# Optimization experiments

Measured on AMD Instinct MI355X. Metric: run time of the kernel, lower is better.

Reference implementation:

```python
import jax, jax.numpy as jnp
import numpy as np

N_EMBD = 2048
N_HEAD = 32
N_GROUPS = 8
HEAD_DIM = N_EMBD // N_HEAD
Q_PER_KV = N_HEAD // N_GROUPS
QKV_DIM = (Q_PER_KV + 2) * N_GROUPS * HEAD_DIM


def apply_rope(x, cos, sin):
    # x: [B, nH, T, hd]; cos/sin: [T, rot//2]
    B, nH, T, hd = x.shape
    rot = min(sin.shape[1] * 2, hd)
    half = rot // 2
    x_rot, x_pass = x[..., :rot], x[..., rot:]
    c = cos[:T, :half][None, None]  # [1,1,T,half]
    s = sin[:T, :half][None, None]
    x1, x2 = x_rot[..., :half], x_rot[..., half:]
    x1_ = x1 * c - x2 * s
    x2_ = x2 * c + x1 * s
    return jnp.concatenate([x1_, x2_, x_pass], axis=-1)


def setup_inputs() -> dict:
    key = jax.random.key(0)
    k1, k2, k3, k4, k5 = jax.random.split(key, 5)
    B, T = 2, 2048
    x = jax.random.normal(k1, (B, T, N_EMBD), dtype=jnp.float32)
    cos = jax.random.uniform(k2, (T, HEAD_DIM // 2), dtype=jnp.float32)
    sin = jax.random.uniform(k3, (T, HEAD_DIM // 2), dtype=jnp.float32)
    attn_w = jax.random.normal(k4, (QKV_DIM, N_EMBD), dtype=jnp.float32) * (1.0 / np.sqrt(N_EMBD))
    proj_w = jax.random.normal(k5, (N_EMBD, N_EMBD), dtype=jnp.float32) * (1.0 / np.sqrt(N_EMBD))
    return {"x": x, "cos": cos, "sin": sin, "attn_w": attn_w, "proj_w": proj_w}


def reference(x, cos, sin, attn_w, proj_w):
    B, T, E = x.shape
    qkv = jnp.einsum('bte,fe->btf', x, attn_w)  # [B,T,QKV_DIM]
    qkv = qkv.reshape(B, T, N_GROUPS, Q_PER_KV + 2, HEAD_DIM)
    q = qkv[:, :, :, :Q_PER_KV].reshape(B, T, N_HEAD, HEAD_DIM)
    k = qkv[:, :, :, Q_PER_KV]      # [B,T,G,hd]
    v = qkv[:, :, :, Q_PER_KV + 1]  # [B,T,G,hd]
    # [B, heads, T, hd] layout; GQA repeat_interleave of K/V to full head count
    q = q.transpose(0, 2, 1, 3)
    k = jnp.repeat(k.transpose(0, 2, 1, 3), Q_PER_KV, axis=1)
    v = jnp.repeat(v.transpose(0, 2, 1, 3), Q_PER_KV, axis=1)
    q = apply_rope(q, cos, sin)
    k = apply_rope(k, cos, sin)
    scale = 1.0 / np.sqrt(HEAD_DIM)
    att = jax.nn.softmax(jnp.einsum('bhqd,bhkd->bhqk', q, k) * scale, axis=-1)
    out = jnp.einsum('bhqk,bhkd->bhqd', att, v)  # [B,nH,T,hd]
    out = out.transpose(0, 2, 1, 3).reshape(B, T, N_HEAD * HEAD_DIM)
    return jnp.einsum('bte,fe->btf', out, proj_w)
```

## Files before the change

kernel.cpp:

```cpp
#include <hip/hip_runtime.h>

typedef unsigned short u16;
typedef unsigned int u32;
typedef __bf16 bf16x8 __attribute__((ext_vector_type(8)));
typedef float f32x4 __attribute__((ext_vector_type(4)));
typedef float f32x16 __attribute__((ext_vector_type(16)));
typedef unsigned int u32x4 __attribute__((ext_vector_type(4)));

__device__ __forceinline__ u16 f2bf(float f) {
    u32 u = __builtin_bit_cast(u32, f);
    u32 r = u + 0x7FFFu + ((u >> 16) & 1u);
    return (u16)(r >> 16);
}
__device__ __forceinline__ u32 pack_bf16(float v0, float v1) {
    u32 a = __builtin_bit_cast(u32, v0) + 0x8000u;
    u32 b = __builtin_bit_cast(u32, v1) + 0x8000u;
    return __builtin_amdgcn_perm(b, a, 0x07060302u);
}
__device__ __forceinline__ u32 cvtpk(float lo, float hi) {
    u32 r;
    asm("v_cvt_pk_bf16_f32 %0, %1, %2" : "=v"(r) : "v"(lo), "v"(hi));
    return r;
}
__device__ __forceinline__ void plswap(u32& a, u32& b) {
    asm("v_permlane32_swap_b32 %0, %1" : "+v"(a), "+v"(b));
}
__device__ __forceinline__ void gload16(const u16* g, u16* l) {
    __builtin_amdgcn_global_load_lds(
        (const __attribute__((address_space(1))) u32*)g,
        (__attribute__((address_space(3))) u32*)l, 16, 0, 0);
}

#define QSCALE 0.18033688011111793f


__global__ __launch_bounds__(256) void cvt3_kernel(const float* __restrict__ a, u16* __restrict__ ao,
                                                   const float* __restrict__ b, u16* __restrict__ bo,
                                                   const float* __restrict__ c, u16* __restrict__ co) {
    int i = blockIdx.x * 256 + threadIdx.x;
    const float* src; u16* dst; int idx;
    if (i < 2097152)       { src = a; dst = ao; idx = i; }
    else if (i < 3670016)  { src = b; dst = bo; idx = i - 2097152; }
    else                   { src = c; dst = co; idx = i - 3670016; }
    float4 f = reinterpret_cast<const float4*>(src)[idx];
    u32 lo = (u32)f2bf(f.x) | ((u32)f2bf(f.y) << 16);
    u32 hi = (u32)f2bf(f.z) | ((u32)f2bf(f.w) << 16);
    reinterpret_cast<uint2*>(dst)[idx] = make_uint2(lo, hi);
}

__global__ __launch_bounds__(512, 2) void gemm_qkv(const u16* __restrict__ A,
                                                   const u16* __restrict__ Bw,
                                                   const float* __restrict__ cosb,
                                                   const float* __restrict__ sinb,
                                                   u16* __restrict__ Qo,
                                                   u16* __restrict__ Ko,
                                                   u16* __restrict__ Vt) {
    __shared__ __align__(16) u16 As[2 * 2 * 128 * 64];
    __shared__ __align__(16) u16 Bs[2 * 2 * 128 * 64];
    const int tid = threadIdx.x;
    const int w = tid >> 6, lane = tid & 63;
    const int quad = lane >> 4, l15 = lane & 15;
    const int wr = w >> 2, wc = w & 3;
    const int m0 = blockIdx.x * 256, n0 = blockIdx.y * 256;
    const int K = 2048;
    const int rsub = lane >> 3;
    const int csrc = (lane & 7) ^ rsub;
    const int sx = (l15 & 7) << 3;
    const int c0 = (quad * 8) ^ sx;
    const int c1 = (32 + quad * 8) ^ sx;

    f32x4 acc[8][4];
#pragma unroll
    for (int a = 0; a < 8; a++)
#pragma unroll
        for (int b = 0; b < 4; b++) acc[a][b] = (f32x4){0.f, 0.f, 0.f, 0.f};

    auto stage = [&](const u16* g, int row0, int kk, u16* lds) {
#pragma unroll
        for (int i = 0; i < 2; i++)
            gload16(g + (size_t)(row0 + (i * 8 + w) * 8 + rsub) * K + kk + csrc * 8,
                    lds + (i * 8 + w) * 512);
    };

    stage(A,  m0,       0, &As[0]);
    stage(A,  m0 + 128, 0, &As[8192]);
    stage(Bw, n0,       0, &Bs[0]);
    stage(Bw, n0 + 128, 0, &Bs[8192]);
    asm volatile("s_waitcnt vmcnt(0)" ::: "memory");
    __builtin_amdgcn_s_barrier();

    for (int j = 0; j < 32; ++j) {
        const int cur = j & 1;
        const u16* Ab = &As[cur * 16384 + wr * 8192];
        const u16* Bb = &Bs[cur * 16384 + (wc >> 1) * 8192 + (wc & 1) * 4096];
        u16* Asn = &As[(cur ^ 1) * 16384];
        u16* Bsn = &Bs[(cur ^ 1) * 16384];
        const int kk2 = (j + 1) * 64;
        bf16x8 af[4][2];
#pragma unroll
        for (int q = 0; q < 4; ++q) {
            const int qm = q >> 1, qn = q & 1;
            if (qn == 0) {
#pragma unroll
                for (int fm = 0; fm < 4; fm++) {
                    af[fm][0] = *reinterpret_cast<const bf16x8*>(&Ab[(qm * 64 + fm * 16 + l15) * 64 + c0]);
                    af[fm][1] = *reinterpret_cast<const bf16x8*>(&Ab[(qm * 64 + fm * 16 + l15) * 64 + c1]);
                }
            }
            bf16x8 bfv[2][2];
#pragma unroll
            for (int fn = 0; fn < 2; fn++) {
                bfv[fn][0] = *reinterpret_cast<const bf16x8*>(&Bb[(qn * 32 + fn * 16 + l15) * 64 + c0]);
                bfv[fn][1] = *reinterpret_cast<const bf16x8*>(&Bb[(qn * 32 + fn * 16 + l15) * 64 + c1]);
            }
            if (j < 31) {
                if (q == 0)      { stage(A,  m0,       kk2, Asn); stage(A,  m0 + 128, kk2, Asn + 8192); }
                else if (q == 1) { stage(Bw, n0,       kk2, Bsn); stage(Bw, n0 + 128, kk2, Bsn + 8192); }
            }
            __builtin_amdgcn_s_barrier();
            __builtin_amdgcn_s_setprio(1);
#pragma unroll
            for (int fm = 0; fm < 4; fm++)
#pragma unroll
                for (int fn = 0; fn < 2; fn++) {
                    acc[qm * 4 + fm][qn * 2 + fn] = __builtin_amdgcn_mfma_f32_16x16x32_bf16(
                        af[fm][0], bfv[fn][0], acc[qm * 4 + fm][qn * 2 + fn], 0, 0, 0);
                    acc[qm * 4 + fm][qn * 2 + fn] = __builtin_amdgcn_mfma_f32_16x16x32_bf16(
                        af[fm][1], bfv[fn][1], acc[qm * 4 + fm][qn * 2 + fn], 0, 0, 0);
                }
            __builtin_amdgcn_s_setprio(0);
            if (q == 3 && j < 31) asm volatile("s_waitcnt vmcnt(0)" ::: "memory");
            __builtin_amdgcn_s_barrier();
        }
    }

    const int nw0 = n0 + wc * 64;
    const int G = nw0 / 384;
    const int slot = (nw0 % 384) / 64;
    const int bb = m0 >> 11;
    const int tb0 = (m0 & 2047) + wr * 128 + quad * 4;
    if (slot == 5) {
        u16* vbase = Vt + ((size_t)(bb * 8 + G)) * 131072;
        const int half_v = quad >> 1, jb = (quad & 1) * 4;
#pragma unroll
        for (int fm = 0; fm < 8; fm++) {
            const int trow = tb0 + fm * 16;
            const int sb = (trow >> 6) * 4096 + ((trow >> 4) & 3) * 512 + half_v * 256 + jb;
#pragma unroll
            for (int fn = 0; fn < 4; fn++) {
                const int dt = fn >> 1, dl = (fn & 1) * 16 + l15;
                uint2 pk;
                pk.x = pack_bf16(acc[fm][fn][0], acc[fm][fn][1]);
                pk.y = pack_bf16(acc[fm][fn][2], acc[fm][fn][3]);
                *reinterpret_cast<uint2*>(vbase + sb + dt * 2048 + dl * 8) = pk;
            }
        }
    } else {
        const float sc = (slot < 4) ? QSCALE : 1.0f;
        u16* obase = (slot < 4)
            ? Qo + ((size_t)(bb * 32 + G * 4 + slot)) * 131072
            : Ko + ((size_t)(bb * 8 + G)) * 131072;
        const int laneoff = (l15 >> 3) * 256 + (l15 & 7);
#pragma unroll
        for (int fm = 0; fm < 8; fm++) {
#pragma unroll
            for (int i = 0; i < 4; i++) {
                const int t = tb0 + fm * 16 + i;
                const int tb = (t >> 5) * 2048 + (t & 31) * 8 + laneoff;
#pragma unroll
                for (int fn = 0; fn < 2; fn++) {
                    const int dh = fn * 16 + l15;
                    float c = cosb[t * 32 + dh], s = sinb[t * 32 + dh];
                    float x1 = acc[fm][fn][i], x2 = acc[fm][fn + 2][i];
                    obase[tb + fn * 512]       = f2bf((x1 * c - x2 * s) * sc);
                    obase[tb + (fn + 2) * 512] = f2bf((x2 * c + x1 * s) * sc);
                }
            }
        }
    }
}

__global__ __launch_bounds__(256) void gemm_bt(const u16* __restrict__ A,
                                               const u16* __restrict__ Bw,
                                               float* __restrict__ Cf,
                                               int M, int N, int K) {
    __shared__ __align__(16) u16 As[2 * 128 * 32];
    __shared__ __align__(16) u16 Bs[2 * 128 * 32];
    const int tid = threadIdx.x;
    const int wave = tid >> 6, lane = tid & 63, quad = lane >> 4, l15 = lane & 15;
    const int wm = wave >> 1, wn = wave & 1;
    const int m0 = blockIdx.x * 128, n0 = blockIdx.y * 128;
    const int lrow = lane >> 2, lcol = (lane & 3) * 8;
    f32x4 acc[4][4];
#pragma unroll
    for (int a = 0; a < 4; a++)
#pragma unroll
        for (int b = 0; b < 4; b++) acc[a][b] = (f32x4){0.f, 0.f, 0.f, 0.f};
    for (int kk = 0; kk < K; kk += 64) {
        __syncthreads();
#pragma unroll
        for (int p = 0; p < 2; p++)
#pragma unroll
            for (int c = 0; c < 2; c++) {
                const int rA = wave * 32 + c * 16;
                gload16(A  + (size_t)(m0 + rA + lrow) * K + kk + p * 32 + lcol,
                        &As[p * 4096 + rA * 32]);
                gload16(Bw + (size_t)(n0 + rA + lrow) * K + kk + p * 32 + lcol,
                        &Bs[p * 4096 + rA * 32]);
            }
        __syncthreads();
#pragma unroll
        for (int p = 0; p < 2; p++) {
            bf16x8 af[4], bfr[4];
#pragma unroll
            for (int t = 0; t < 4; t++) {
                af[t]  = *reinterpret_cast<const bf16x8*>(
                    &As[p * 4096 + (wm * 64 + t * 16 + l15) * 32 + quad * 8]);
                bfr[t] = *reinterpret_cast<const bf16x8*>(
                    &Bs[p * 4096 + (wn * 64 + t * 16 + l15) * 32 + quad * 8]);
            }
#pragma unroll
            for (int tm = 0; tm < 4; tm++)
#pragma unroll
                for (int tn = 0; tn < 4; tn++)
                    acc[tm][tn] = __builtin_amdgcn_mfma_f32_16x16x32_bf16(af[tm], bfr[tn], acc[tm][tn], 0, 0, 0);
        }
    }
#pragma unroll
    for (int tm = 0; tm < 4; tm++) {
        const int r0 = m0 + wm * 64 + tm * 16 + quad * 4;
#pragma unroll
        for (int tn = 0; tn < 4; tn++) {
            const int c = n0 + wn * 64 + tn * 16 + l15;
#pragma unroll
            for (int i = 0; i < 4; i++) Cf[(size_t)(r0 + i) * N + c] = acc[tm][tn][i];
        }
    }
}

__global__ __launch_bounds__(256, 4) void attn(const u16* __restrict__ Q,
                                               const u16* __restrict__ Kg,
                                               const u16* __restrict__ Vt,
                                               u16* __restrict__ O) {
    __shared__ __align__(16) u16 Ks[3 * 4096];
    __shared__ __align__(16) u16 Vts[2 * 4096];
    const int tid = threadIdx.x, w = tid >> 6, lane = tid & 63;
    const int half = lane >> 5, l31 = lane & 31;
    const int q0 = blockIdx.x * 128;
    const int h = blockIdx.y, b = blockIdx.z, g = h >> 2;
    const u16* qfb = Q + ((size_t)(b * 32 + h)) * 131072;
    const u16* kfb = Kg + ((size_t)(b * 8 + g)) * 131072;
    const u16* vfb = Vt + ((size_t)(b * 8 + g)) * 131072;

    const int Tq = (q0 >> 6) + (w >> 1);
#pragma unroll
    for (int ks = 0; ks < 4; ks++)
        gload16(qfb + ((size_t)((Tq * 8 + (w & 1) * 4 + ks) * 64) + lane) * 8,
                Ks + (w * 4 + ks) * 512);
    __syncthreads();
    bf16x8 qf[4];
#pragma unroll
    for (int ks = 0; ks < 4; ks++)
        qf[ks] = *reinterpret_cast<const bf16x8*>(&Ks[(w * 4 + ks) * 512 + lane * 8]);
    __syncthreads();

    f32x16 Oa[2];
#pragma unroll
    for (int t = 0; t < 2; t++)
#pragma unroll
        for (int i = 0; i < 16; i++) Oa[t][i] = 0.f;
    float lsum = 0.f;

    auto stage_k = [&](int T, int bsel) {
        u16* kd = Ks + bsel * 4096;
#pragma unroll
        for (int i = 0; i < 2; i++) {
            const int s = w * 2 + i;
            gload16(kfb + ((size_t)((T * 8 + s) * 64) + lane) * 8, kd + s * 512);
        }
    };
    auto stage_v = [&](int T, int bsel) {
        u16* vd = Vts + bsel * 4096;
#pragma unroll
        for (int i = 0; i < 2; i++) {
            const int s = w * 2 + i;
            gload16(vfb + ((size_t)((T * 8 + s) * 64) + lane) * 8, vd + s * 512);
        }
    };
    auto qk = [&](f32x16 (&S)[2], const u16* Kb) {
#pragma unroll
        for (int kt = 0; kt < 2; kt++) {
#pragma unroll
            for (int i = 0; i < 16; i++) S[kt][i] = 0.f;
#pragma unroll
            for (int ks = 0; ks < 4; ks++) {
                bf16x8 kf = *reinterpret_cast<const bf16x8*>(&Kb[(kt * 4 + ks) * 512 + lane * 8]);
                S[kt] = __builtin_amdgcn_mfma_f32_32x32x16_bf16(kf, qf[ks], S[kt], 0, 0, 0);
            }
        }
    };

    stage_k(0, 0);
    stage_v(0, 0);
    stage_k(1, 1);
    __syncthreads();
    f32x16 Sa[2], Sb[2];
    __builtin_amdgcn_s_setprio(1);
    qk(Sa, Ks);
    __builtin_amdgcn_s_setprio(0);

    auto body = [&](int t, int bn, int bs, f32x16 (&Sc)[2], f32x16 (&Sn)[2],
                    const u16* Vb) {
        if (t < 31) stage_v(t + 1, (t + 1) & 1);
        if (t < 30) stage_k(t + 2, bs);
        float ps = 0.f;
        u32 pw[4][4];
#pragma unroll
        for (int kt = 0; kt < 2; kt++) {
            float pe[16];
#pragma unroll
            for (int r = 0; r < 16; r++) pe[r] = __builtin_amdgcn_exp2f(Sc[kt][r]);
#pragma unroll
            for (int r = 0; r < 4; r++)
                ps += (pe[r * 4 + 0] + pe[r * 4 + 1]) + (pe[r * 4 + 2] + pe[r * 4 + 3]);
#pragma unroll
            for (int j = 0; j < 2; j++) {
                u32 X0 = cvtpk(pe[j * 8 + 0], pe[j * 8 + 1]);
                u32 Y0 = cvtpk(pe[j * 8 + 4], pe[j * 8 + 5]);
                u32 X1 = cvtpk(pe[j * 8 + 2], pe[j * 8 + 3]);
                u32 Y1 = cvtpk(pe[j * 8 + 6], pe[j * 8 + 7]);
                plswap(X0, Y0);
                plswap(X1, Y1);
                const int ks2 = kt * 2 + j;
                pw[ks2][0] = X0; pw[ks2][1] = X1; pw[ks2][2] = Y0; pw[ks2][3] = Y1;
            }
        }
        __builtin_amdgcn_s_setprio(1);
        qk(Sn, Ks + bn * 4096);
#pragma unroll
        for (int ks2 = 0; ks2 < 4; ks2++) {
            u32x4 pv = (u32x4){pw[ks2][0], pw[ks2][1], pw[ks2][2], pw[ks2][3]};
            bf16x8 pf = __builtin_bit_cast(bf16x8, pv);
#pragma unroll
            for (int dt = 0; dt < 2; dt++) {
                bf16x8 vf = *reinterpret_cast<const bf16x8*>(
                    &Vb[(dt * 4 + ks2) * 512 + lane * 8]);
                Oa[dt] = __builtin_amdgcn_mfma_f32_32x32x16_bf16(vf, pf, Oa[dt], 0, 0, 0);
            }
        }
        __builtin_amdgcn_s_setprio(0);
        lsum += ps;
        __syncthreads();
    };

    int b0 = 0, b1 = 1, b2 = 2;
    for (int k2 = 0; k2 < 16; ++k2) {
        const int t0 = k2 * 2;
        body(t0,     b1, b2, Sa, Sb, Vts);
        body(t0 + 1, b2, b0, Sb, Sa, Vts + 4096);
        const int nb0 = b2, nb1 = b0, nb2 = b1;
        b0 = nb0; b1 = nb1; b2 = nb2;
    }

    float lt = lsum + __shfl_xor(lsum, 32);
    float linv = 1.f / lt;
    const int t = q0 + w * 32 + l31;
    u16* orow = O + ((size_t)(b * 2048 + t)) * 2048 + h * 64;
#pragma unroll
    for (int dt = 0; dt < 2; dt++)
#pragma unroll
        for (int gr = 0; gr < 4; gr++) {
            uint2 pk;
            pk.x = pack_bf16(Oa[dt][gr * 4 + 0] * linv, Oa[dt][gr * 4 + 1] * linv);
            pk.y = pack_bf16(Oa[dt][gr * 4 + 2] * linv, Oa[dt][gr * 4 + 3] * linv);
            *reinterpret_cast<uint2*>(orow + dt * 32 + 8 * gr + 4 * half) = pk;
        }
}

extern "C" void kernel_launch(void* const* d_in, const int* in_sizes, int n_in,
                              void* d_out, int out_size, void* d_ws, size_t ws_size,
                              hipStream_t stream) {
    const float* x      = (const float*)d_in[0];
    const float* cosb   = (const float*)d_in[1];
    const float* sinb   = (const float*)d_in[2];
    const float* attn_w = (const float*)d_in[3];
    const float* proj_w = (const float*)d_in[4];
    float* out = (float*)d_out;

    u16* xb  = (u16*)d_ws;
    u16* w1b = xb  + (size_t)4096 * 2048;
    u16* w2b = w1b + (size_t)3072 * 2048;
    u16* qo  = w2b + (size_t)2048 * 2048;
    u16* ko  = qo  + (size_t)2 * 32 * 2048 * 64;
    u16* vt  = ko  + (size_t)2 * 8 * 2048 * 64;
    u16* ao  = xb;

    cvt3_kernel<<<18432, 256, 0, stream>>>(x, xb, attn_w, w1b, proj_w, w2b);
    gemm_qkv<<<dim3(16, 12), 512, 0, stream>>>(xb, w1b, cosb, sinb, qo, ko, vt);
    attn<<<dim3(16, 32, 2), 256, 0, stream>>>(qo, ko, vt, ao);
    gemm_bt<<<dim3(32, 16), 256, 0, stream>>>(ao, w2b, out, 4096, 2048, 2048);
}
```

Before: 314.8 us.

## Restructure output projection GEMM with double-buffered swizzled LDS and larger tiles

```diff
diff --git a/kernel.cpp b/kernel.cpp
--- a/kernel.cpp
+++ b/kernel.cpp
@@ -180,58 +180,95 @@
     }
 }
 
-__global__ __launch_bounds__(256) void gemm_bt(const u16* __restrict__ A,
-                                               const u16* __restrict__ Bw,
-                                               float* __restrict__ Cf,
-                                               int M, int N, int K) {
-    __shared__ __align__(16) u16 As[2 * 128 * 32];
-    __shared__ __align__(16) u16 Bs[2 * 128 * 32];
+__global__ __launch_bounds__(512, 2) void gemm_bt(const u16* __restrict__ A,
+                                                  const u16* __restrict__ Bw,
+                                                  float* __restrict__ Cf,
+                                                  int M, int N, int K) {
+    __shared__ __align__(16) u16 As[2 * 128 * 64];
+    __shared__ __align__(16) u16 Bs[2 * 2 * 128 * 64];
     const int tid = threadIdx.x;
-    const int wave = tid >> 6, lane = tid & 63, quad = lane >> 4, l15 = lane & 15;
-    const int wm = wave >> 1, wn = wave & 1;
-    const int m0 = blockIdx.x * 128, n0 = blockIdx.y * 128;
-    const int lrow = lane >> 2, lcol = (lane & 3) * 8;
+    const int w = tid >> 6, lane = tid & 63;
+    const int quad = lane >> 4, l15 = lane & 15;
+    const int wr = w >> 2, wc = w & 3;
+    const int m0 = blockIdx.x * 128, n0 = blockIdx.y * 256;
+    const int rsub = lane >> 3;
+    const int csrc = (lane & 7) ^ rsub;
+    const int sx = (l15 & 7) << 3;
+    const int c0 = (quad * 8) ^ sx;
+    const int c1 = (32 + quad * 8) ^ sx;
+
     f32x4 acc[4][4];
 #pragma unroll
     for (int a = 0; a < 4; a++)
 #pragma unroll
         for (int b = 0; b < 4; b++) acc[a][b] = (f32x4){0.f, 0.f, 0.f, 0.f};
-    for (int kk = 0; kk < K; kk += 64) {
-        __syncthreads();
-#pragma unroll
-        for (int p = 0; p < 2; p++)
-#pragma unroll
-            for (int c = 0; c < 2; c++) {
-                const int rA = wave * 32 + c * 16;
-                gload16(A  + (size_t)(m0 + rA + lrow) * K + kk + p * 32 + lcol,
-                        &As[p * 4096 + rA * 32]);
-                gload16(Bw + (size_t)(n0 + rA + lrow) * K + kk + p * 32 + lcol,
-                        &Bs[p * 4096 + rA * 32]);
-            }
-        __syncthreads();
-#pragma unroll
-        for (int p = 0; p < 2; p++) {
-            bf16x8 af[4], bfr[4];
-#pragma unroll
-            for (int t = 0; t < 4; t++) {
-                af[t]  = *reinterpret_cast<const bf16x8*>(
-                    &As[p * 4096 + (wm * 64 + t * 16 + l15) * 32 + quad * 8]);
-                bfr[t] = *reinterpret_cast<const bf16x8*>(
-                    &Bs[p * 4096 + (wn * 64 + t * 16 + l15) * 32 + quad * 8]);
-            }
-#pragma unroll
-            for (int tm = 0; tm < 4; tm++)
-#pragma unroll
-                for (int tn = 0; tn < 4; tn++)
-                    acc[tm][tn] = __builtin_amdgcn_mfma_f32_16x16x32_bf16(af[tm], bfr[tn], acc[tm][tn], 0, 0, 0);
+
+    auto stage = [&](const u16* g, int row0, int kk, u16* lds) {
+#pragma unroll
+        for (int i = 0; i < 2; i++)
+            gload16(g + (size_t)(row0 + (i * 8 + w) * 8 + rsub) * K + kk + csrc * 8,
+                    lds + (i * 8 + w) * 512);
+    };
+
+    stage(A,  m0,       0, &As[0]);
+    stage(Bw, n0,       0, &Bs[0]);
+    stage(Bw, n0 + 128, 0, &Bs[8192]);
+    asm volatile("s_waitcnt vmcnt(0)" ::: "memory");
+    __builtin_amdgcn_s_barrier();
+
+    const int nt = K >> 6;
+    for (int j = 0; j < nt; ++j) {
+        const int cur = j & 1;
+        const u16* Ab = &As[cur * 8192];
+        const u16* Bb = &Bs[cur * 16384 + (wc >> 1) * 8192 + (wc & 1) * 4096];
+        u16* Asn = &As[(cur ^ 1) * 8192];
+        u16* Bsn = &Bs[(cur ^ 1) * 16384];
+        const int kk2 = (j + 1) * 64;
+        bf16x8 af[2][2];
+#pragma unroll
+        for (int q = 0; q < 4; ++q) {
+            const int qm = q >> 1, qn = q & 1;
+            if (qn == 0) {
+#pragma unroll
+                for (int fm = 0; fm < 2; fm++) {
+                    const int r = wr * 64 + (qm * 2 + fm) * 16 + l15;
+                    af[fm][0] = *reinterpret_cast<const bf16x8*>(&Ab[r * 64 + c0]);
+                    af[fm][1] = *reinterpret_cast<const bf16x8*>(&Ab[r * 64 + c1]);
+                }
+            }
+            bf16x8 bfv[2][2];
+#pragma unroll
+            for (int fn = 0; fn < 2; fn++) {
+                bfv[fn][0] = *reinterpret_cast<const bf16x8*>(&Bb[(qn * 32 + fn * 16 + l15) * 64 + c0]);
+                bfv[fn][1] = *reinterpret_cast<const bf16x8*>(&Bb[(qn * 32 + fn * 16 + l15) * 64 + c1]);
+            }
+            if (j < nt - 1) {
+                if (q == 0)      stage(A,  m0, kk2, Asn);
+                else if (q == 1) { stage(Bw, n0, kk2, Bsn); stage(Bw, n0 + 128, kk2, Bsn + 8192); }
+            }
+            __builtin_amdgcn_s_barrier();
+            __builtin_amdgcn_s_setprio(1);
+#pragma unroll
+            for (int fm = 0; fm < 2; fm++)
+#pragma unroll
+                for (int fn = 0; fn < 2; fn++) {
+                    acc[qm * 2 + fm][qn * 2 + fn] = __builtin_amdgcn_mfma_f32_16x16x32_bf16(
+                        af[fm][0], bfv[fn][0], acc[qm * 2 + fm][qn * 2 + fn], 0, 0, 0);
+                    acc[qm * 2 + fm][qn * 2 + fn] = __builtin_amdgcn_mfma_f32_16x16x32_bf16(
+                        af[fm][1], bfv[fn][1], acc[qm * 2 + fm][qn * 2 + fn], 0, 0, 0);
+                }
+            __builtin_amdgcn_s_setprio(0);
+            if (q == 3 && j < nt - 1) asm volatile("s_waitcnt vmcnt(0)" ::: "memory");
+            __builtin_amdgcn_s_barrier();
         }
     }
+
 #pragma unroll
     for (int tm = 0; tm < 4; tm++) {
-        const int r0 = m0 + wm * 64 + tm * 16 + quad * 4;
+        const int r0 = m0 + wr * 64 + tm * 16 + quad * 4;
 #pragma unroll
         for (int tn = 0; tn < 4; tn++) {
-            const int c = n0 + wn * 64 + tn * 16 + l15;
+            const int c = n0 + wc * 64 + tn * 16 + l15;
 #pragma unroll
             for (int i = 0; i < 4; i++) Cf[(size_t)(r0 + i) * N + c] = acc[tm][tn][i];
         }
@@ -398,5 +435,5 @@
     cvt3_kernel<<<18432, 256, 0, stream>>>(x, xb, attn_w, w1b, proj_w, w2b);
     gemm_qkv<<<dim3(16, 12), 512, 0, stream>>>(xb, w1b, cosb, sinb, qo, ko, vt);
     attn<<<dim3(16, 32, 2), 256, 0, stream>>>(qo, ko, vt, ao);
-    gemm_bt<<<dim3(32, 16), 256, 0, stream>>>(ao, w2b, out, 4096, 2048, 2048);
-}
+    gemm_bt<<<dim3(32, 8), 512, 0, stream>>>(ao, w2b, out, 4096, 2048, 2048);
+}
```

New measurement: 311.3 us. About the same (-1.1%).
